# Performance work log

Measured on AMD Instinct MI355X. Metric: run time of the kernel, lower is better.

Reference implementation:

```python
import jax, jax.numpy as jnp
import numpy as np

C = 100      # number of classes
B = 1024     # buffer_size
D = 768      # backbone feature_dim
N = 8192     # number of samples
CHUNK = 32   # scan chunk for outer-product scatter-add


def setup_inputs() -> dict:
    key = jax.random.key(0)
    k1, k2, k3 = jax.random.split(key, 3)
    X = jax.random.normal(k1, (N, D), dtype=jnp.float32)
    W = jax.random.normal(k2, (D, B), dtype=jnp.float32) / np.sqrt(D).astype(np.float32)
    labels = jax.random.randint(k3, (N,), 0, C, dtype=jnp.int32)
    return {"X": X, "W": W, "labels": labels}


def reference(X, W, labels):
    # RandomBuffer projection: relu(X @ W)  -> [N, B]
    feat = jax.nn.relu(X @ W)

    # Label-bucketed accumulation of per-sample outer products f^T @ f into
    # per-class covariance buffers (the fit() hot loop), vectorized as a
    # chunked scatter-add instead of a Python per-sample loop.
    feat_c = feat.reshape(N // CHUNK, CHUNK, B)
    lab_c = labels.reshape(N // CHUNK, CHUNK)

    def body(phi, inp):
        f, lab = inp                                  # f: [CHUNK, B]
        outer = jnp.einsum('ni,nj->nij', f, f)        # [CHUNK, B, B]
        return phi.at[lab].add(outer), None

    phi0 = jnp.zeros((C, B, B), dtype=jnp.float32)
    phi, _ = jax.lax.scan(body, phi0, (feat_c, lab_c))

    # temp_mu[label] += f ; temp_count[label] += 1
    mu = jax.ops.segment_sum(feat, labels, num_segments=C)                 # [C, B]
    counts = jax.ops.segment_sum(jnp.ones((N,), jnp.float32), labels,
                                 num_segments=C)                           # [C]
    return phi, mu, counts
```

## Files before the change

kernel.cpp:

```cpp
#include <hip/hip_runtime.h>
#include <hip/hip_bf16.h>

#define CNUM 100
#define NS   8192
#define DIM  768
#define BF   1024
#define SP   12288
#define PHI_SZ ((size_t)CNUM * BF * BF)
#define MU_SZ  ((size_t)CNUM * BF)

typedef float f32x4 __attribute__((ext_vector_type(4)));
typedef short s16x8 __attribute__((ext_vector_type(8)));

#define GL2LDS(gp, lp) __builtin_amdgcn_global_load_lds( \
    (const __attribute__((address_space(1))) void*)(gp), \
    (__attribute__((address_space(3))) void*)(lp), 16, 0, 0)

#define WAITV4 do { asm volatile("s_waitcnt vmcnt(4)" ::: "memory"); } while (0)
#define WAITV0 do { asm volatile("s_waitcnt vmcnt(0)" ::: "memory"); } while (0)

static __device__ __forceinline__ unsigned short f2bf(float x) {
  union { float f; unsigned int u; } v; v.f = x;
  unsigned int lsb = (v.u >> 16) & 1;
  v.u += 0x7fffu + lsb;
  return (unsigned short)(v.u >> 16);
}

static __device__ __forceinline__ float bf2f(unsigned short u) {
  return __uint_as_float(((unsigned int)u) << 16);
}

#define NCVT (NS * DIM / 4 / 256)
#define NWT  ((DIM / 32) * (BF / 32))


__global__ __launch_bounds__(256) void k_cvt(
    const float* __restrict__ X, unsigned short* __restrict__ Xbf,
    const float* __restrict__ W, unsigned short* __restrict__ WT,
    const int* __restrict__ lab, int* __restrict__ sIdx, int* __restrict__ poff,
    float* __restrict__ outCounts, unsigned short* __restrict__ zeroPad)
{
  __shared__ union {
    float tile[32][33];
    struct { int hw[4][104]; int wb[4][104]; int rk[4][104]; int off[CNUM + 1]; } p;
  } sm;
  const int b = blockIdx.x;
  const int t = threadIdx.x;
  if (b == 0) {
    const int w = t >> 6, l = t & 63;
    for (int i = t; i < 4 * 104; i += 256) { (&sm.p.hw[0][0])[i] = 0; (&sm.p.rk[0][0])[i] = 0; }
    __syncthreads();
    int myLab[32];
#pragma unroll
    for (int p = 0; p < 32; ++p)
      myLab[p] = lab[w * 2048 + p * 64 + l];
#pragma unroll
    for (int p = 0; p < 32; ++p)
      atomicAdd(&sm.p.hw[w][myLab[p]], 1);
    for (int i = t; i < SP; i += 256) sIdx[i] = -1;
    for (int i = t; i < DIM; i += 256) zeroPad[i] = 0;
    __syncthreads();
    if (t < CNUM) {
      int base = 0;
#pragma unroll
      for (int ww = 0; ww < 4; ++ww) { sm.p.wb[ww][t] = base; base += sm.p.hw[ww][t]; }
      sm.p.hw[0][t] = base;
    }
    __syncthreads();
    if (t == 0) {
      int a = 0;
      for (int c = 0; c < CNUM; ++c) { sm.p.off[c] = a; a += (sm.p.hw[0][c] + 31) & ~31; }
      sm.p.off[CNUM] = a;
    }
    __syncthreads();
    if (t < CNUM) outCounts[t] = (float)sm.p.hw[0][t];
    if (t <= CNUM) poff[t] = sm.p.off[t];
#pragma unroll
    for (int p = 0; p < 32; ++p) {
      const int n = w * 2048 + p * 64 + l;
      const int c = myLab[p];
      const int r = atomicAdd(&sm.p.rk[w][c], 1);
      sIdx[sm.p.off[c] + sm.p.wb[w][c] + r] = n;
    }
  } else if (b <= NCVT) {
    size_t i = ((size_t)(b - 1) * 256 + t) * 4;
    float4 v = *(const float4*)(X + i);
    *(ushort4*)(Xbf + i) = make_ushort4(f2bf(v.x), f2bf(v.y), f2bf(v.z), f2bf(v.w));
  } else {
    const int bb = b - 1 - NCVT;
    const int kb = (bb % (DIM / 32)) * 32;
    const int fb = (bb / (DIM / 32)) * 32;
    {
      const int cc = t & 31, r4 = t >> 5;
#pragma unroll
      for (int i = 0; i < 4; ++i) {
        int r = r4 * 4 + i;
        sm.tile[r][cc] = W[(size_t)(kb + r) * BF + fb + cc];
      }
    }
    __syncthreads();
    {
      const int kc = t & 31, f4 = t >> 5;
#pragma unroll
      for (int i = 0; i < 4; ++i) {
        int fr = f4 * 4 + i;
        WT[(size_t)(fb + fr) * DIM + kb + kc] = f2bf(sm.tile[kc][fr]);
      }
    }
  }
}


__global__ __launch_bounds__(256) void k_gemm1(
    const unsigned short* __restrict__ Xbf,
    const unsigned short* __restrict__ WT,
    const int* __restrict__ sIdx,
    const unsigned short* __restrict__ zeroPad,
    unsigned short* __restrict__ featT)
{
  __shared__ __align__(16) unsigned short As[2][128][32];
  __shared__ __align__(16) unsigned short Bs[2][128][32];

  const int t = threadIdx.x;
  const int bid = blockIdx.x;
  const int o = (bid & 7) * 96 + (bid >> 3);
  const int f0 = (o & 7) * 128;
  const int s0 = (o >> 3) * 128;
  const int lane = t & 63;
  const int wave = t >> 6;
  const int wr = wave >> 1, wc = wave & 1;

  const int rr = t >> 2, qp = t & 3;
  const int rA0 = rr, rA1 = 64 + rr;
  const int qg0 = qp ^ ((rA0 >> 1) & 3);
  const int qg1 = qp ^ ((rA1 >> 1) & 3);
  const int n0 = sIdx[s0 + rA0];
  const int n1 = sIdx[s0 + rA1];
  const unsigned short* aSrc0 = (n0 >= 0 ? Xbf + (size_t)n0 * DIM : zeroPad) + qg0 * 8;
  const unsigned short* aSrc1 = (n1 >= 0 ? Xbf + (size_t)n1 * DIM : zeroPad) + qg1 * 8;
  const unsigned short* bSrc0 = WT + (size_t)(f0 + rA0) * DIM + qg0 * 8;
  const unsigned short* bSrc1 = WT + (size_t)(f0 + rA1) * DIM + qg1 * 8;
  unsigned short* aD = &As[0][0][0] + t * 8;
  unsigned short* bD = &Bs[0][0][0] + t * 8;

#define STAGE1(buf, kt) do {                      \
    const int o2 = (kt) * 32;                     \
    unsigned short* ad = aD + (buf) * 4096;       \
    unsigned short* bd = bD + (buf) * 4096;       \
    GL2LDS(aSrc0 + o2, ad);                       \
    GL2LDS(aSrc1 + o2, ad + 2048);                \
    GL2LDS(bSrc0 + o2, bd);                       \
    GL2LDS(bSrc1 + o2, bd + 2048);                \
  } while (0)

  f32x4 acc[4][4];
#pragma unroll
  for (int m = 0; m < 4; ++m)
#pragma unroll
    for (int q = 0; q < 4; ++q) acc[m][q] = (f32x4)0.0f;

  STAGE1(0, 0);
  STAGE1(1, 1);
  int cur = 0;
  for (int kt = 0; kt < DIM / 32; ++kt) {
    if (kt + 1 < DIM / 32) WAITV4; else WAITV0;
    __builtin_amdgcn_sched_barrier(0);
    __builtin_amdgcn_s_barrier();

    s16x8 a[4], b[4];
#pragma unroll
    for (int m = 0; m < 4; ++m) {
      const int row = wr * 64 + m * 16 + (lane & 15);
      const int sq = (lane >> 4) ^ ((row >> 1) & 3);
      a[m] = *(const s16x8*)((const char*)As + cur * 8192 + row * 64 + sq * 16);
    }
#pragma unroll
    for (int q = 0; q < 4; ++q) {
      const int row = wc * 64 + q * 16 + (lane & 15);
      const int sq = (lane >> 4) ^ ((row >> 1) & 3);
      b[q] = *(const s16x8*)((const char*)Bs + cur * 8192 + row * 64 + sq * 16);
    }
#pragma unroll
    for (int m = 0; m < 4; ++m)
#pragma unroll
      for (int q = 0; q < 4; ++q)
        acc[m][q] = __builtin_amdgcn_mfma_f32_16x16x32_bf16(a[m], b[q], acc[m][q], 0, 0, 0);

    __builtin_amdgcn_sched_barrier(0);
    __builtin_amdgcn_s_barrier();
    if (kt + 2 < DIM / 32) STAGE1(cur, kt + 2);
    cur ^= 1;
  }

  const int rbase = s0 + wr * 64 + ((lane >> 4) << 2);
  const int cbase = f0 + wc * 64 + (lane & 15);
#pragma unroll
  for (int m = 0; m < 4; ++m) {
#pragma unroll
    for (int q = 0; q < 4; ++q) {
      f32x4 v = acc[m][q];
      unsigned short p0 = f2bf(fmaxf(v[0], 0.f));
      unsigned short p1 = f2bf(fmaxf(v[1], 0.f));
      unsigned short p2 = f2bf(fmaxf(v[2], 0.f));
      unsigned short p3 = f2bf(fmaxf(v[3], 0.f));
      const int s = rbase + m * 16;
      const int f = cbase + q * 16;
      *(ushort4*)(featT + (size_t)f * SP + s) = make_ushort4(p0, p1, p2, p3);
    }
  }
}


#define NMU 1600

__global__ __launch_bounds__(256) void k_phimu(
    const unsigned short* __restrict__ featT,
    const int* __restrict__ poff,
    float* __restrict__ out, float* __restrict__ mu)
{
  const int bid = blockIdx.x;
  const int t = threadIdx.x;
  const int lane = t & 63;
  const int wave = t >> 6;

  if (bid < NMU) {
    const int c = bid % CNUM;
    const int bx = bid / CNUM;
    const int k0 = poff[c], k1 = poff[c + 1];
#pragma unroll 1
    for (int i = 0; i < 16; ++i) {
      const int f = bx * 64 + wave * 16 + i;
      float s = 0.f;
      for (int b = k0 + lane; b < k1; b += 64)
        s += bf2f(featT[(size_t)f * SP + b]);
#pragma unroll
      for (int off = 32; off > 0; off >>= 1) s += __shfl_down(s, off, 64);
      if (lane == 0) mu[(size_t)c * BF + f] = s;
    }
    return;
  }

  __shared__ __align__(16) char smem[32768];
  unsigned short* AsB = (unsigned short*)smem;
  unsigned short* BsB = (unsigned short*)(smem + 16384);
  float (*tbuf)[132] = (float(*)[132])smem;

  const int sid = bid - NMU;
  const int o = (sid & 7) * 800 + (sid >> 3);
  const int c = o >> 6;
  const int t64 = o & 63;
  const int i0 = (t64 >> 3) * 128;
  const int j0 = (t64 & 7) * 128;
  const int wr = wave >> 1, wc = wave & 1;

  const int kb0 = poff[c];
  const int ksteps = (poff[c + 1] - kb0) >> 5;

  const int rr = t >> 2, qp = t & 3;
  const int rA0 = rr, rA1 = 64 + rr;
  const int qg0 = qp ^ ((rA0 >> 1) & 3);
  const int qg1 = qp ^ ((rA1 >> 1) & 3);
  const unsigned short* aSrc0 = featT + (size_t)(i0 + rA0) * SP + kb0 + qg0 * 8;
  const unsigned short* aSrc1 = featT + (size_t)(i0 + rA1) * SP + kb0 + qg1 * 8;
  const unsigned short* bSrc0 = featT + (size_t)(j0 + rA0) * SP + kb0 + qg0 * 8;
  const unsigned short* bSrc1 = featT + (size_t)(j0 + rA1) * SP + kb0 + qg1 * 8;
  unsigned short* aD = AsB + t * 8;
  unsigned short* bD = BsB + t * 8;

#define STAGE2(buf, kt) do {                      \
    const int o2 = (kt) * 32;                     \
    unsigned short* ad = aD + (buf) * 4096;       \
    unsigned short* bd = bD + (buf) * 4096;       \
    GL2LDS(aSrc0 + o2, ad);                       \
    GL2LDS(aSrc1 + o2, ad + 2048);                \
    GL2LDS(bSrc0 + o2, bd);                       \
    GL2LDS(bSrc1 + o2, bd + 2048);                \
  } while (0)

  f32x4 acc[4][4];
#pragma unroll
  for (int m = 0; m < 4; ++m)
#pragma unroll
    for (int q = 0; q < 4; ++q) acc[m][q] = (f32x4)0.0f;

  if (ksteps > 0) STAGE2(0, 0);
  if (ksteps > 1) STAGE2(1, 1);
  int cur = 0;
#pragma unroll 1
  for (int kt = 0; kt < ksteps; ++kt) {
    if (kt + 1 < ksteps) WAITV4; else WAITV0;
    __builtin_amdgcn_sched_barrier(0);
    __builtin_amdgcn_s_barrier();

    s16x8 a[4], b[4];
#pragma unroll
    for (int m = 0; m < 4; ++m) {
      const int row = wr * 64 + m * 16 + (lane & 15);
      const int sq = (lane >> 4) ^ ((row >> 1) & 3);
      a[m] = *(const s16x8*)((const char*)AsB + cur * 8192 + row * 64 + sq * 16);
    }
#pragma unroll
    for (int q = 0; q < 4; ++q) {
      const int row = wc * 64 + q * 16 + (lane & 15);
      const int sq = (lane >> 4) ^ ((row >> 1) & 3);
      b[q] = *(const s16x8*)((const char*)BsB + cur * 8192 + row * 64 + sq * 16);
    }
#pragma unroll
    for (int m = 0; m < 4; ++m)
#pragma unroll
      for (int q = 0; q < 4; ++q)
        acc[m][q] = __builtin_amdgcn_mfma_f32_16x16x32_bf16(a[m], b[q], acc[m][q], 0, 0, 0);

    __builtin_amdgcn_sched_barrier(0);
    __builtin_amdgcn_s_barrier();
    if (kt + 2 < ksteps) STAGE2(cur, kt + 2);
    cur ^= 1;
  }

  float* phiC = out + (size_t)c * (BF * BF);
  const int s4   = (lane >> 4) << 2;
  const int lrow = wr * 16 + s4;
  const int lcol = wc * 64 + (lane & 15);
  const int rcol = (t & 31) * 4;
  const int rr8  = t >> 5;
#pragma unroll
  for (int m = 0; m < 4; ++m) {
    __syncthreads();
#pragma unroll
    for (int q = 0; q < 4; ++q) {
      f32x4 v = acc[m][q];
#pragma unroll
      for (int r = 0; r < 4; ++r)
        tbuf[lrow + r][lcol + q * 16] = v[r];
    }
    __syncthreads();
#pragma unroll
    for (int u = 0; u < 4; ++u) {
      const int r = u * 8 + rr8;
      const int grow = i0 + (r >> 4) * 64 + m * 16 + (r & 15);
      f32x4 val = *(const f32x4*)&tbuf[r][rcol];
      __builtin_nontemporal_store(val, (f32x4*)(phiC + (size_t)grow * BF + j0 + rcol));
    }
  }
}


extern "C" void kernel_launch(void* const* d_in, const int* in_sizes, int n_in,
                              void* d_out, int out_size, void* d_ws, size_t ws_size,
                              hipStream_t stream) {
  const float* X = (const float*)d_in[0];
  const float* W = (const float*)d_in[1];
  const int* lab = (const int*)d_in[2];
  float* out = (float*)d_out;
  char* ws = (char*)d_ws;

  int* poff = (int*)(ws);
  int* sIdx = (int*)(ws + 1024);
  unsigned short* zeroPad = (unsigned short*)(ws + 1024 + SP * 4);
  unsigned short* featT = (unsigned short*)(ws + 65536);
  unsigned short* Xbf = (unsigned short*)(ws + 65536 + (size_t)BF * SP * 2);
  unsigned short* WT  = (unsigned short*)(ws + 65536 + (size_t)BF * SP * 2 + (size_t)NS * DIM * 2);

  k_cvt<<<1 + NCVT + NWT, 256, 0, stream>>>(X, Xbf, W, WT, lab, sIdx, poff,
                                            out + PHI_SZ + MU_SZ, zeroPad);
  k_gemm1<<<768, 256, 0, stream>>>(Xbf, WT, sIdx, zeroPad, featT);
  k_phimu<<<NMU + CNUM * 64, 256, 0, stream>>>(featT, poff, out, out + (size_t)PHI_SZ);
}
```

Baseline: 126.4 us.

## Fuse per-class mu reduction into diagonal phi tiles and use nontemporal X loads

Removes the 1600 separate mu-reduction blocks and instead has the diagonal 128x128 phi tiles sum their staged A rows from LDS during the K loop, writing mu directly. This avoids rereading featT from global memory for mu and shrinks the grid. The trade-off is extra LDS reads and adds on diagonal blocks, which makes them slightly slower than the others. The X-to-bf16 conversion also switches to nontemporal loads.

```diff
diff --git a/kernel.cpp b/kernel.cpp
--- a/kernel.cpp
+++ b/kernel.cpp
@@ -84,8 +84,8 @@
     }
   } else if (b <= NCVT) {
     size_t i = ((size_t)(b - 1) * 256 + t) * 4;
-    float4 v = *(const float4*)(X + i);
-    *(ushort4*)(Xbf + i) = make_ushort4(f2bf(v.x), f2bf(v.y), f2bf(v.z), f2bf(v.w));
+    f32x4 v = __builtin_nontemporal_load((const f32x4*)(X + i));
+    *(ushort4*)(Xbf + i) = make_ushort4(f2bf(v[0]), f2bf(v[1]), f2bf(v[2]), f2bf(v[3]));
   } else {
     const int bb = b - 1 - NCVT;
     const int kb = (bb % (DIM / 32)) * 32;
@@ -211,9 +211,9 @@
 }
 
 
-#define NMU 1600
-
-__global__ __launch_bounds__(256) void k_phimu(
+#define NPHI (CNUM * 64)
+
+__global__ __launch_bounds__(256) void k_phi(
     const unsigned short* __restrict__ featT,
     const int* __restrict__ poff,
     float* __restrict__ out, float* __restrict__ mu)
@@ -223,34 +223,17 @@
   const int lane = t & 63;
   const int wave = t >> 6;
 
-  if (bid < NMU) {
-    const int c = bid % CNUM;
-    const int bx = bid / CNUM;
-    const int k0 = poff[c], k1 = poff[c + 1];
-#pragma unroll 1
-    for (int i = 0; i < 16; ++i) {
-      const int f = bx * 64 + wave * 16 + i;
-      float s = 0.f;
-      for (int b = k0 + lane; b < k1; b += 64)
-        s += bf2f(featT[(size_t)f * SP + b]);
-#pragma unroll
-      for (int off = 32; off > 0; off >>= 1) s += __shfl_down(s, off, 64);
-      if (lane == 0) mu[(size_t)c * BF + f] = s;
-    }
-    return;
-  }
-
   __shared__ __align__(16) char smem[32768];
   unsigned short* AsB = (unsigned short*)smem;
   unsigned short* BsB = (unsigned short*)(smem + 16384);
   float (*tbuf)[132] = (float(*)[132])smem;
 
-  const int sid = bid - NMU;
-  const int o = (sid & 7) * 800 + (sid >> 3);
+  const int o = (bid & 7) * 800 + (bid >> 3);
   const int c = o >> 6;
   const int t64 = o & 63;
   const int i0 = (t64 >> 3) * 128;
   const int j0 = (t64 & 7) * 128;
+  const bool diag = (t64 >> 3) == (t64 & 7);
   const int wr = wave >> 1, wc = wave & 1;
 
   const int kb0 = poff[c];
@@ -283,6 +266,10 @@
 #pragma unroll
     for (int q = 0; q < 4; ++q) acc[m][q] = (f32x4)0.0f;
 
+  float msum = 0.f;
+  const int mrow = t >> 1;
+  const int mhalf = t & 1;
+
   if (ksteps > 0) STAGE2(0, 0);
   if (ksteps > 1) STAGE2(1, 1);
   int cur = 0;
@@ -311,10 +298,24 @@
       for (int q = 0; q < 4; ++q)
         acc[m][q] = __builtin_amdgcn_mfma_f32_16x16x32_bf16(a[m], b[q], acc[m][q], 0, 0, 0);
 
+    if (diag) {
+      const char* rbp = (const char*)AsB + cur * 8192 + mrow * 64 + mhalf * 32;
+      s16x8 u0 = *(const s16x8*)rbp;
+      s16x8 u1 = *(const s16x8*)(rbp + 16);
+#pragma unroll
+      for (int e = 0; e < 8; ++e)
+        msum += bf2f((unsigned short)u0[e]) + bf2f((unsigned short)u1[e]);
+    }
+
     __builtin_amdgcn_sched_barrier(0);
     __builtin_amdgcn_s_barrier();
     if (kt + 2 < ksteps) STAGE2(cur, kt + 2);
     cur ^= 1;
+  }
+
+  if (diag) {
+    const float other = __shfl_xor(msum, 1, 64);
+    if (mhalf == 0) mu[(size_t)c * BF + i0 + mrow] = msum + other;
   }
 
   float* phiC = out + (size_t)c * (BF * BF);
@@ -364,5 +365,5 @@
   k_cvt<<<1 + NCVT + NWT, 256, 0, stream>>>(X, Xbf, W, WT, lab, sIdx, poff,
                                             out + PHI_SZ + MU_SZ, zeroPad);
   k_gemm1<<<768, 256, 0, stream>>>(Xbf, WT, sIdx, zeroPad, featT);
-  k_phimu<<<NMU + CNUM * 64, 256, 0, stream>>>(featT, poff, out, out + (size_t)PHI_SZ);
-}
+  k_phi<<<NPHI, 256, 0, stream>>>(featT, poff, out, out + (size_t)PHI_SZ);
+}
```

After: 117.2 us (median of 2 runs). -7.2%, faster.
